# Optimization experiments

Hardware: AMD Instinct MI355X
Metric: run time of the kernel (lower is better)

## Reference

```python
import jax, jax.numpy as jnp
import numpy as np

N_TOKENS = 16384
DIM = 2048
N_EXPERTS = 64
TOPK = 8
ROUTE_SCALE = 1.0


def setup_inputs() -> dict:
    key = jax.random.key(0)
    k1, k2 = jax.random.split(key)
    x = jax.random.normal(k1, (N_TOKENS, DIM), dtype=jnp.float32)
    W = jax.random.normal(k2, (N_EXPERTS, DIM), dtype=jnp.float32) * 0.02
    return {"x": x, "W": W}


def reference(x, W):
    # linear scores: [tokens, n_experts]
    logits = jnp.einsum('td,ed->te', x, W)
    # softmax in float32 (score_func == 'softmax'); bias is None since dim != 64
    scores = jax.nn.softmax(logits.astype(jnp.float32), axis=-1)
    # top-k expert selection, then gather original scores at selected indices
    _, indices = jax.lax.top_k(scores, TOPK)
    weights = jnp.take_along_axis(scores, indices, axis=-1)
    # softmax path: no renormalization, just route scaling
    weights = (weights * ROUTE_SCALE).astype(x.dtype)
    return weights, indices
```

## Files before the change

kernel.cpp:

```cpp
#include <hip/hip_runtime.h>


typedef __attribute__((ext_vector_type(8))) short short8;
typedef __attribute__((ext_vector_type(16))) float f32x16;
typedef __attribute__((ext_vector_type(4))) float f32x4;
typedef __attribute__((ext_vector_type(4))) unsigned int u32x4;

#define NT    16384
#define DIMK  2048
#define NE    64
#define TOPKK 8
#define WPK_BYTES 786432
#define PL_BYTES  (4 * NT * NE * 4)
#define WS_NEED   (WPK_BYTES + PL_BYTES)

union U4S8 { unsigned int u[4]; short8 s; u32x4 v; };

__device__ __forceinline__ short8 as_s8(u32x4 v) { U4S8 t; t.v = v; return t.s; }

__device__ __forceinline__ void split3(const float4 a, const float4 b,
                                       short8& H, short8& M, short8& L) {
    const float f[8] = {a.x, a.y, a.z, a.w, b.x, b.y, b.z, b.w};
    U4S8 uh, um, ul;
#pragma unroll
    for (int p = 0; p < 4; ++p) {
        const float f0 = f[2 * p], f1 = f[2 * p + 1];
        const unsigned int t0 = __float_as_uint(f0) & 0xFFFF0000u;
        const unsigned int t1 = __float_as_uint(f1) & 0xFFFF0000u;
        uh.u[p] = (t0 >> 16) | t1;
        const float r0 = f0 - __uint_as_float(t0);
        const float r1 = f1 - __uint_as_float(t1);
        const unsigned int v0 = __float_as_uint(r0) & 0xFFFF0000u;
        const unsigned int v1 = __float_as_uint(r1) & 0xFFFF0000u;
        um.u[p] = (v0 >> 16) | v1;
        const float s0 = r0 - __uint_as_float(v0);
        const float s1 = r1 - __uint_as_float(v1);
        ul.u[p] = (__float_as_uint(s0) >> 16) | (__float_as_uint(s1) & 0xFFFF0000u);
    }
    H = uh.s; M = um.s; L = ul.s;
}

__device__ __forceinline__ f32x16 mfma6w(short8 ah, short8 am, short8 al,
                                         short8 bh, short8 bm, short8 bl,
                                         f32x16 c) {
    c = __builtin_amdgcn_mfma_f32_32x32x16_bf16(ah, bh, c, 0, 0, 0);
    c = __builtin_amdgcn_mfma_f32_32x32x16_bf16(ah, bm, c, 0, 0, 0);
    c = __builtin_amdgcn_mfma_f32_32x32x16_bf16(am, bh, c, 0, 0, 0);
    c = __builtin_amdgcn_mfma_f32_32x32x16_bf16(ah, bl, c, 0, 0, 0);
    c = __builtin_amdgcn_mfma_f32_32x32x16_bf16(am, bm, c, 0, 0, 0);
    c = __builtin_amdgcn_mfma_f32_32x32x16_bf16(al, bh, c, 0, 0, 0);
    return c;
}

__global__ __launch_bounds__(64) void pack_w_kernel(
    const float* __restrict__ W, short* __restrict__ wpk)
{
    const int b  = blockIdx.x;
    const int c  = b >> 3, fg = b & 7;
    const int s  = fg >> 1, n32 = fg & 1;
    const int l  = threadIdx.x;
    const float* g = W + (size_t)(32 * n32 + (l & 31)) * DIMK
                       + 64 * c + 16 * s + 8 * (l >> 5);
    const float4 lo = *(const float4*)g;
    const float4 hi = *(const float4*)(g + 4);
    short8 H, M, L;
    split3(lo, hi, H, M, L);
    const size_t base = ((size_t)(c * 8 + fg) * 3) * 512 + l * 8;
    *(short8*)(wpk + base)        = H;
    *(short8*)(wpk + base + 512)  = M;
    *(short8*)(wpk + base + 1024) = L;
}

#define WLOAD3(d0, d1, d2, p)                                                 \
    asm volatile("global_load_dwordx4 %0, %3, off\n\t"                        \
                 "global_load_dwordx4 %1, %3, off offset:1024\n\t"            \
                 "global_load_dwordx4 %2, %3, off offset:2048"                \
                 : "=&v"(d0), "=&v"(d1), "=&v"(d2) : "v"(p))
#define WAITN(n) do {                                                         \
    asm volatile("s_waitcnt vmcnt(" #n ")" ::: "memory");                     \
    __builtin_amdgcn_sched_barrier(0);                                        \
} while (0)

__device__ __forceinline__ void async16nt(void* lds, const void* gp) {
    __builtin_amdgcn_global_load_lds(
        (const __attribute__((address_space(1))) unsigned int*)gp,
        (__attribute__((address_space(3))) unsigned int*)lds, 16, 0, 2 );
}

__global__ __launch_bounds__(512, 1) void gate_ksplit_kernel(
    const float* __restrict__ x, const short* __restrict__ wpk,
    float* __restrict__ pl)
{
    __shared__ __align__(16) char smem[8 * 3 * 4096];

    const int tid = threadIdx.x;
    const int w   = tid >> 6;
    const int l   = tid & 63;
    const int r31 = l & 31;
    const int l5  = l >> 5;
    const int tg  = blockIdx.x >> 2;
    const int kq  = blockIdx.x & 3;
    const int bt0 = tg * 256;
    const int tokbase = bt0 + 32 * w;

    char* wbase = smem + w * 12288;
    const int swr = (r31 & 7) ^ (((r31 >> 3) & 3) << 1);
    const int srow = l >> 3;
    const int sg0  = (l & 7) ^ srow;
    const float* xrow0 = x + (size_t)(tokbase + srow) * DIMK + kq * 512;

#define STAGE_CHUNK(k) do {                                                   \
    _Pragma("unroll")                                                         \
    for (int i = 0; i < 4; ++i) {                                             \
        const float* gsrc = xrow0 + (size_t)(8 * i) * DIMK + (k) * 32         \
                          + ((sg0 ^ (2 * i)) << 2);                           \
        async16nt(wbase + ((k) % 3) * 4096 + i * 1024, gsrc);                 \
    }                                                                         \
} while (0)

    const short* wq0 = wpk + (size_t)kq * 98304 + l * 8;
    const short* wq1 = wq0 + 1536;

    f32x16 acc0, acc1;
#pragma unroll
    for (int i = 0; i < 16; ++i) { acc0[i] = 0.f; acc1[i] = 0.f; }

    u32x4 w0v[4][3], w1v[4][3];

    STAGE_CHUNK(0);
    STAGE_CHUNK(1);
    STAGE_CHUNK(2);
    WLOAD3(w0v[0][0], w0v[0][1], w0v[0][2], wq0); wq0 += 3072;
    WLOAD3(w1v[0][0], w1v[0][1], w1v[0][2], wq1); wq1 += 3072;
    WLOAD3(w0v[1][0], w0v[1][1], w0v[1][2], wq0); wq0 += 3072;
    WLOAD3(w1v[1][0], w1v[1][1], w1v[1][2], wq1); wq1 += 3072;
    WLOAD3(w0v[2][0], w0v[2][1], w0v[2][2], wq0); wq0 += 3072;
    WLOAD3(w1v[2][0], w1v[2][1], w1v[2][2], wq1); wq1 += 3072;

#define SLICE(t) do {                                                         \
    if ((t) <= 28) {                                                          \
        WLOAD3(w0v[((t)+3)&3][0], w0v[((t)+3)&3][1], w0v[((t)+3)&3][2], wq0); \
        wq0 += 3072;                                                          \
        WLOAD3(w1v[((t)+3)&3][0], w1v[((t)+3)&3][1], w1v[((t)+3)&3][2], wq1); \
        wq1 += 3072;                                                          \
    }                                                                         \
    if ((t) <= 1)            WAITN(18);                                       \
    else if ((t) == 29)      WAITN(12);                                       \
    else if ((t) == 30)      WAITN(6);                                        \
    else if ((t) == 31)      WAITN(0);                                        \
    else if (((t) & 1) || (t) == 2 || (t) == 28) WAITN(22);                   \
    else                     WAITN(26);                                       \
    {                                                                         \
        const char* xb = wbase + (((t) >> 1) % 3) * 4096;                     \
        const float4 a0 = *(const float4*)(xb + r31 * 128 +                   \
            (((((t) & 1) * 4 + 2 * l5 + 0) ^ swr) << 4));                     \
        const float4 a1 = *(const float4*)(xb + r31 * 128 +                   \
            (((((t) & 1) * 4 + 2 * l5 + 1) ^ swr) << 4));                     \
        short8 H, M, L;                                                       \
        split3(a0, a1, H, M, L);                                              \
        acc0 = mfma6w(H, M, L, as_s8(w0v[(t)&3][0]), as_s8(w0v[(t)&3][1]),    \
                      as_s8(w0v[(t)&3][2]), acc0);                            \
        acc1 = mfma6w(H, M, L, as_s8(w1v[(t)&3][0]), as_s8(w1v[(t)&3][1]),    \
                      as_s8(w1v[(t)&3][2]), acc1);                            \
    }                                                                         \
    if (((t) & 1) && (t) <= 25) STAGE_CHUNK(((t) + 5) >> 1);                  \
} while (0)

#define PBAR() __builtin_amdgcn_s_barrier()

    SLICE(0);  SLICE(1);  SLICE(2);  SLICE(3);  PBAR();
    SLICE(4);  SLICE(5);  SLICE(6);  SLICE(7);  PBAR();
    SLICE(8);  SLICE(9);  SLICE(10); SLICE(11); PBAR();
    SLICE(12); SLICE(13); SLICE(14); SLICE(15); PBAR();
    SLICE(16); SLICE(17); SLICE(18); SLICE(19); PBAR();
    SLICE(20); SLICE(21); SLICE(22); SLICE(23); PBAR();
    SLICE(24); SLICE(25); SLICE(26); SLICE(27); PBAR();
    SLICE(28); SLICE(29); SLICE(30); SLICE(31);

    float* base0 = pl + ((size_t)kq * NT + tokbase) * NE;
#pragma unroll
    for (int r = 0; r < 16; ++r) {
        const int rowc = (r & 3) + 8 * (r >> 2) + 4 * l5;
        base0[rowc * NE + r31]      = acc0[r];
        base0[rowc * NE + 32 + r31] = acc1[r];
    }
#undef SLICE
#undef STAGE_CHUNK
#undef PBAR
}

__global__ __launch_bounds__(64) void gate_combine_kernel(
    const float* __restrict__ pl, float* __restrict__ out)
{
    const int g = blockIdx.x * 64 + threadIdx.x;
    const f32x4* p0 = (const f32x4*)(pl + (size_t)g * NE);
    const f32x4* p1 = (const f32x4*)(pl + ((size_t)NT + g) * NE);
    const f32x4* p2 = (const f32x4*)(pl + ((size_t)2 * NT + g) * NE);
    const f32x4* p3 = (const f32x4*)(pl + ((size_t)3 * NT + g) * NE);

    f32x4 row[16];
#pragma unroll
    for (int j = 0; j < 16; ++j)
        row[j] = (p0[j] + p1[j]) + (p2[j] + p3[j]);

    float mx = -3.402823466e38f;
#pragma unroll
    for (int j = 0; j < 16; ++j)
#pragma unroll
        for (int c = 0; c < 4; ++c) mx = fmaxf(mx, row[j][c]);

    float sden = 0.f;
#pragma unroll
    for (int j = 0; j < 16; ++j)
#pragma unroll
        for (int c = 0; c < 4; ++c) sden += expf(row[j][c] - mx);

    float tv[TOPKK];
    int   ti[TOPKK];
#pragma unroll
    for (int i = 0; i < TOPKK; ++i) { tv[i] = -3.402823466e38f; ti[i] = 0; }
#pragma unroll
    for (int j = 0; j < 16; ++j)
#pragma unroll
        for (int c = 0; c < 4; ++c) {
            const float v = row[j][c];
            const int   e = 4 * j + c;
            if (v > tv[TOPKK - 1]) {
                tv[TOPKK - 1] = v; ti[TOPKK - 1] = e;
#pragma unroll
                for (int q = TOPKK - 1; q > 0; --q) {
                    if (tv[q] > tv[q - 1]) {
                        const float fv = tv[q]; tv[q] = tv[q - 1]; tv[q - 1] = fv;
                        const int   iv = ti[q]; ti[q] = ti[q - 1]; ti[q - 1] = iv;
                    }
                }
            }
        }

    float* ow = out + (size_t)g * TOPKK;
    float* oi = out + (size_t)NT * TOPKK + (size_t)g * TOPKK;
#pragma unroll
    for (int i = 0; i < TOPKK; ++i) {
        ow[i] = expf(tv[i] - mx) / sden;
        oi[i] = (float)ti[i];
    }
}

__device__ __forceinline__ void async16(void* lds, const void* gp) {
    __builtin_amdgcn_global_load_lds(
        (const __attribute__((address_space(1))) unsigned int*)gp,
        (__attribute__((address_space(3))) unsigned int*)lds, 16, 0, 0);
}

__global__ __launch_bounds__(512, 1) void gate_main_r8(
    const float* __restrict__ x, const short* __restrict__ wpk,
    float* __restrict__ out)
{
    __shared__ __align__(16) char smem[8 * 3 * 4096];
    const int tid = threadIdx.x;
    const int w   = tid >> 6;
    const int l   = tid & 63;
    const int r31 = l & 31;
    const int l5  = l >> 5;
    const int tw  = w & 1;
    const int kq  = w >> 1;
    const int bt0 = blockIdx.x * 64;
    char* wbase = smem + w * 12288;
    const int swr = (r31 & 7) ^ (((r31 >> 3) & 3) << 1);
    const int srow = l >> 3;
    const int sg0  = (l & 7) ^ srow;
    const float* xrow0 = x + (size_t)(bt0 + 32 * tw + srow) * DIMK + kq * 512;

#define STAGE_CHUNK(k) do {                                                   \
    _Pragma("unroll")                                                         \
    for (int i = 0; i < 4; ++i) {                                             \
        const float* gsrc = xrow0 + (size_t)(8 * i) * DIMK + (k) * 32         \
                          + ((sg0 ^ (2 * i)) << 2);                           \
        async16(wbase + ((k) % 3) * 4096 + i * 1024, gsrc);                   \
    }                                                                         \
} while (0)

    const short* wq0 = wpk + (size_t)kq * 98304 + l * 8;
    const short* wq1 = wq0 + 1536;
    f32x16 acc0, acc1;
#pragma unroll
    for (int i = 0; i < 16; ++i) { acc0[i] = 0.f; acc1[i] = 0.f; }
    u32x4 w0v[4][3], w1v[4][3];
    STAGE_CHUNK(0); STAGE_CHUNK(1); STAGE_CHUNK(2);
    WLOAD3(w0v[0][0], w0v[0][1], w0v[0][2], wq0); wq0 += 3072;
    WLOAD3(w1v[0][0], w1v[0][1], w1v[0][2], wq1); wq1 += 3072;
    WLOAD3(w0v[1][0], w0v[1][1], w0v[1][2], wq0); wq0 += 3072;
    WLOAD3(w1v[1][0], w1v[1][1], w1v[1][2], wq1); wq1 += 3072;
    WLOAD3(w0v[2][0], w0v[2][1], w0v[2][2], wq0); wq0 += 3072;
    WLOAD3(w1v[2][0], w1v[2][1], w1v[2][2], wq1); wq1 += 3072;

#define SLICE(t) do {                                                         \
    if ((t) <= 28) {                                                          \
        WLOAD3(w0v[((t)+3)&3][0], w0v[((t)+3)&3][1], w0v[((t)+3)&3][2], wq0); \
        wq0 += 3072;                                                          \
        WLOAD3(w1v[((t)+3)&3][0], w1v[((t)+3)&3][1], w1v[((t)+3)&3][2], wq1); \
        wq1 += 3072;                                                          \
    }                                                                         \
    if ((t) <= 1)            WAITN(18);                                       \
    else if ((t) == 29)      WAITN(12);                                       \
    else if ((t) == 30)      WAITN(6);                                        \
    else if ((t) == 31)      WAITN(0);                                        \
    else if (((t) & 1) || (t) == 2 || (t) == 28) WAITN(22);                   \
    else                     WAITN(26);                                       \
    {                                                                         \
        const char* xb = wbase + (((t) >> 1) % 3) * 4096;                     \
        const float4 a0 = *(const float4*)(xb + r31 * 128 +                   \
            (((((t) & 1) * 4 + 2 * l5 + 0) ^ swr) << 4));                     \
        const float4 a1 = *(const float4*)(xb + r31 * 128 +                   \
            (((((t) & 1) * 4 + 2 * l5 + 1) ^ swr) << 4));                     \
        short8 H, M, L;                                                       \
        split3(a0, a1, H, M, L);                                              \
        acc0 = mfma6w(H, M, L, as_s8(w0v[(t)&3][0]), as_s8(w0v[(t)&3][1]),    \
                      as_s8(w0v[(t)&3][2]), acc0);                            \
        acc1 = mfma6w(H, M, L, as_s8(w1v[(t)&3][0]), as_s8(w1v[(t)&3][1]),    \
                      as_s8(w1v[(t)&3][2]), acc1);                            \
    }                                                                         \
    if (((t) & 1) && (t) <= 25) STAGE_CHUNK(((t) + 5) >> 1);                  \
} while (0)

    SLICE(0);  SLICE(1);  SLICE(2);  SLICE(3);
    SLICE(4);  SLICE(5);  SLICE(6);  SLICE(7);
    SLICE(8);  SLICE(9);  SLICE(10); SLICE(11);
    SLICE(12); SLICE(13); SLICE(14); SLICE(15);
    SLICE(16); SLICE(17); SLICE(18); SLICE(19);
    SLICE(20); SLICE(21); SLICE(22); SLICE(23);
    SLICE(24); SLICE(25); SLICE(26); SLICE(27);
    SLICE(28); SLICE(29); SLICE(30); SLICE(31);

    __syncthreads();
    float* lg = (float*)smem;
#pragma unroll
    for (int r = 0; r < 16; ++r) {
        const int rowc = (r & 3) + 8 * (r >> 2) + 4 * l5;
        const int trow = 32 * tw + rowc;
        lg[(kq * 64 + trow) * (NE + 1) + r31]      = acc0[r];
        lg[(kq * 64 + trow) * (NE + 1) + 32 + r31] = acc1[r];
    }
    __syncthreads();
#pragma unroll
    for (int rr = 0; rr < 8; ++rr) {
        const int idx = tid + rr * 512;
        const int t = idx >> 6, e = idx & 63;
        lg[t * (NE + 1) + e] =
            (lg[t * (NE + 1) + e] + lg[(64 + t) * (NE + 1) + e]) +
            (lg[(128 + t) * (NE + 1) + e] + lg[(192 + t) * (NE + 1) + e]);
    }
    __syncthreads();
    if (tid < 64) {
        const float* rowp = lg + tid * (NE + 1);
        float mx = -3.402823466e38f;
        for (int e = 0; e < NE; ++e) mx = fmaxf(mx, rowp[e]);
        float sden = 0.f;
        for (int e = 0; e < NE; ++e) sden += expf(rowp[e] - mx);
        float tv[TOPKK]; int ti[TOPKK];
#pragma unroll
        for (int i = 0; i < TOPKK; ++i) { tv[i] = -3.402823466e38f; ti[i] = 0; }
        for (int e = 0; e < NE; ++e) {
            const float v = rowp[e];
            if (v > tv[TOPKK - 1]) {
                tv[TOPKK - 1] = v; ti[TOPKK - 1] = e;
#pragma unroll
                for (int q = TOPKK - 1; q > 0; --q) {
                    if (tv[q] > tv[q - 1]) {
                        const float fv = tv[q]; tv[q] = tv[q - 1]; tv[q - 1] = fv;
                        const int   iv = ti[q]; ti[q] = ti[q - 1]; ti[q - 1] = iv;
                    }
                }
            }
        }
        float* ow = out + (size_t)(bt0 + tid) * TOPKK;
        float* oi = out + (size_t)NT * TOPKK + (size_t)(bt0 + tid) * TOPKK;
#pragma unroll
        for (int i = 0; i < TOPKK; ++i) {
            ow[i] = expf(tv[i] - mx) / sden;
            oi[i] = (float)ti[i];
        }
    }
#undef SLICE
#undef STAGE_CHUNK
}

extern "C" void kernel_launch(void* const* d_in, const int* in_sizes, int n_in,
                              void* d_out, int out_size, void* d_ws, size_t ws_size,
                              hipStream_t stream) {
    const float* x = (const float*)d_in[0];
    const float* W = (const float*)d_in[1];
    float* out = (float*)d_out;
    short* wpk = (short*)d_ws;
    if (ws_size >= (size_t)WS_NEED) {
        float* pl = (float*)((char*)d_ws + WPK_BYTES);
        hipLaunchKernelGGL(pack_w_kernel, dim3(256), dim3(64), 0, stream, W, wpk);
        hipLaunchKernelGGL(gate_ksplit_kernel, dim3(256), dim3(512), 0, stream,
                           x, wpk, pl);
        hipLaunchKernelGGL(gate_combine_kernel, dim3(NT / 64), dim3(64), 0, stream,
                           pl, out);
    } else if (ws_size >= (size_t)WPK_BYTES) {
        hipLaunchKernelGGL(pack_w_kernel, dim3(256), dim3(64), 0, stream, W, wpk);
        hipLaunchKernelGGL(gate_main_r8, dim3(NT / 64), dim3(512), 0, stream,
                           x, wpk, out);
    }
}
```

Baseline: 61.63 us.

## Coalesce combine loads via LDS, tighten barriers, drop nontemporal x loads

The combine kernel now loads partial logits cooperatively, with consecutive threads reading consecutive 16-byte chunks, sums the four k-split partials and stages each row in padded LDS before the per-token softmax and top-k. The old version had each thread read whole rows with a large stride, which coalesces poorly. The k-split kernel now places a workgroup barrier every two slices instead of every four, to keep waves in closer lockstep. Its async x loads also drop the nontemporal cache hint. The risks are extra barrier stalls and LDS reads inside the now-rolled per-token loops.

```diff
diff --git a/kernel.cpp b/kernel.cpp
--- a/kernel.cpp
+++ b/kernel.cpp
@@ -81,10 +81,10 @@
     __builtin_amdgcn_sched_barrier(0);                                        \
 } while (0)
 
-__device__ __forceinline__ void async16nt(void* lds, const void* gp) {
+__device__ __forceinline__ void async16(void* lds, const void* gp) {
     __builtin_amdgcn_global_load_lds(
         (const __attribute__((address_space(1))) unsigned int*)gp,
-        (__attribute__((address_space(3))) unsigned int*)lds, 16, 0, 2 );
+        (__attribute__((address_space(3))) unsigned int*)lds, 16, 0, 0);
 }
 
 __global__ __launch_bounds__(512, 1) void gate_ksplit_kernel(
@@ -114,7 +114,7 @@
     for (int i = 0; i < 4; ++i) {                                             \
         const float* gsrc = xrow0 + (size_t)(8 * i) * DIMK + (k) * 32         \
                           + ((sg0 ^ (2 * i)) << 2);                           \
-        async16nt(wbase + ((k) % 3) * 4096 + i * 1024, gsrc);                 \
+        async16(wbase + ((k) % 3) * 4096 + i * 1024, gsrc);                   \
     }                                                                         \
 } while (0)
 
@@ -168,14 +168,22 @@
 
 #define PBAR() __builtin_amdgcn_s_barrier()
 
-    SLICE(0);  SLICE(1);  SLICE(2);  SLICE(3);  PBAR();
-    SLICE(4);  SLICE(5);  SLICE(6);  SLICE(7);  PBAR();
-    SLICE(8);  SLICE(9);  SLICE(10); SLICE(11); PBAR();
-    SLICE(12); SLICE(13); SLICE(14); SLICE(15); PBAR();
-    SLICE(16); SLICE(17); SLICE(18); SLICE(19); PBAR();
-    SLICE(20); SLICE(21); SLICE(22); SLICE(23); PBAR();
-    SLICE(24); SLICE(25); SLICE(26); SLICE(27); PBAR();
-    SLICE(28); SLICE(29); SLICE(30); SLICE(31);
+    SLICE(0);  SLICE(1);  PBAR();
+    SLICE(2);  SLICE(3);  PBAR();
+    SLICE(4);  SLICE(5);  PBAR();
+    SLICE(6);  SLICE(7);  PBAR();
+    SLICE(8);  SLICE(9);  PBAR();
+    SLICE(10); SLICE(11); PBAR();
+    SLICE(12); SLICE(13); PBAR();
+    SLICE(14); SLICE(15); PBAR();
+    SLICE(16); SLICE(17); PBAR();
+    SLICE(18); SLICE(19); PBAR();
+    SLICE(20); SLICE(21); PBAR();
+    SLICE(22); SLICE(23); PBAR();
+    SLICE(24); SLICE(25); PBAR();
+    SLICE(26); SLICE(27); PBAR();
+    SLICE(28); SLICE(29); PBAR();
+    SLICE(30); SLICE(31);
 
     float* base0 = pl + ((size_t)kq * NT + tokbase) * NE;
 #pragma unroll
@@ -189,67 +197,60 @@
 #undef PBAR
 }
 
-__global__ __launch_bounds__(64) void gate_combine_kernel(
+__global__ __launch_bounds__(128) void gate_combine_kernel(
     const float* __restrict__ pl, float* __restrict__ out)
 {
-    const int g = blockIdx.x * 64 + threadIdx.x;
-    const f32x4* p0 = (const f32x4*)(pl + (size_t)g * NE);
-    const f32x4* p1 = (const f32x4*)(pl + ((size_t)NT + g) * NE);
-    const f32x4* p2 = (const f32x4*)(pl + ((size_t)2 * NT + g) * NE);
-    const f32x4* p3 = (const f32x4*)(pl + ((size_t)3 * NT + g) * NE);
-
-    f32x4 row[16];
-#pragma unroll
-    for (int j = 0; j < 16; ++j)
-        row[j] = (p0[j] + p1[j]) + (p2[j] + p3[j]);
-
+    __shared__ float lgs[128][NE + 1];
+
+    const int tid = threadIdx.x;
+    const int t0  = blockIdx.x * 128;
+
+#pragma unroll
+    for (int i = 0; i < 16; ++i) {
+        const int idx = i * 128 + tid;
+        const int tok = idx >> 4, c4 = idx & 15;
+        const size_t off = ((size_t)t0 + tok) * NE + c4 * 4;
+        const f32x4 v0 = *(const f32x4*)(pl + off);
+        const f32x4 v1 = *(const f32x4*)(pl + (size_t)NT * NE + off);
+        const f32x4 v2 = *(const f32x4*)(pl + (size_t)2 * NT * NE + off);
+        const f32x4 v3 = *(const f32x4*)(pl + (size_t)3 * NT * NE + off);
+        const f32x4 s = (v0 + v1) + (v2 + v3);
+#pragma unroll
+        for (int j = 0; j < 4; ++j) lgs[tok][c4 * 4 + j] = s[j];
+    }
+    __syncthreads();
+
+    const float* rowp = &lgs[tid][0];
     float mx = -3.402823466e38f;
-#pragma unroll
-    for (int j = 0; j < 16; ++j)
-#pragma unroll
-        for (int c = 0; c < 4; ++c) mx = fmaxf(mx, row[j][c]);
-
+    for (int e = 0; e < NE; ++e) mx = fmaxf(mx, rowp[e]);
     float sden = 0.f;
-#pragma unroll
-    for (int j = 0; j < 16; ++j)
-#pragma unroll
-        for (int c = 0; c < 4; ++c) sden += expf(row[j][c] - mx);
+    for (int e = 0; e < NE; ++e) sden += expf(rowp[e] - mx);
 
     float tv[TOPKK];
     int   ti[TOPKK];
 #pragma unroll
     for (int i = 0; i < TOPKK; ++i) { tv[i] = -3.402823466e38f; ti[i] = 0; }
-#pragma unroll
-    for (int j = 0; j < 16; ++j)
-#pragma unroll
-        for (int c = 0; c < 4; ++c) {
-            const float v = row[j][c];
-            const int   e = 4 * j + c;
-            if (v > tv[TOPKK - 1]) {
-                tv[TOPKK - 1] = v; ti[TOPKK - 1] = e;
-#pragma unroll
-                for (int q = TOPKK - 1; q > 0; --q) {
-                    if (tv[q] > tv[q - 1]) {
-                        const float fv = tv[q]; tv[q] = tv[q - 1]; tv[q - 1] = fv;
-                        const int   iv = ti[q]; ti[q] = ti[q - 1]; ti[q - 1] = iv;
-                    }
+    for (int e = 0; e < NE; ++e) {
+        const float v = rowp[e];
+        if (v > tv[TOPKK - 1]) {
+            tv[TOPKK - 1] = v; ti[TOPKK - 1] = e;
+#pragma unroll
+            for (int q = TOPKK - 1; q > 0; --q) {
+                if (tv[q] > tv[q - 1]) {
+                    const float fv = tv[q]; tv[q] = tv[q - 1]; tv[q - 1] = fv;
+                    const int   iv = ti[q]; ti[q] = ti[q - 1]; ti[q - 1] = iv;
                 }
             }
         }
-
-    float* ow = out + (size_t)g * TOPKK;
-    float* oi = out + (size_t)NT * TOPKK + (size_t)g * TOPKK;
+    }
+
+    float* ow = out + (size_t)(t0 + tid) * TOPKK;
+    float* oi = out + (size_t)NT * TOPKK + (size_t)(t0 + tid) * TOPKK;
 #pragma unroll
     for (int i = 0; i < TOPKK; ++i) {
         ow[i] = expf(tv[i] - mx) / sden;
         oi[i] = (float)ti[i];
     }
-}
-
-__device__ __forceinline__ void async16(void* lds, const void* gp) {
-    __builtin_amdgcn_global_load_lds(
-        (const __attribute__((address_space(1))) unsigned int*)gp,
-        (__attribute__((address_space(3))) unsigned int*)lds, 16, 0, 0);
 }
 
 __global__ __launch_bounds__(512, 1) void gate_main_r8(
@@ -397,7 +398,7 @@
         hipLaunchKernelGGL(pack_w_kernel, dim3(256), dim3(64), 0, stream, W, wpk);
         hipLaunchKernelGGL(gate_ksplit_kernel, dim3(256), dim3(512), 0, stream,
                            x, wpk, pl);
-        hipLaunchKernelGGL(gate_combine_kernel, dim3(NT / 64), dim3(64), 0, stream,
+        hipLaunchKernelGGL(gate_combine_kernel, dim3(NT / 128), dim3(128), 0, stream,
                            pl, out);
     } else if (ws_size >= (size_t)WPK_BYTES) {
         hipLaunchKernelGGL(pack_w_kernel, dim3(256), dim3(64), 0, stream, W, wpk);
```

Measured after the change: 59.03 us. -4.2%, faster.
